# Performance work log

Hardware: AMD Instinct MI355X
Metric: run time of the kernel (lower is better)

The kernel has to match this reference:

```python
import jax, jax.numpy as jnp
import numpy as np

NEG_SLOPE = 0.01  # nn.LeakyReLU default

def leaky_relu(x):
    return jnp.where(x >= 0, x, NEG_SLOPE * x)

def setup_inputs() -> dict:
    key = jax.random.key(0)
    ks = jax.random.split(key, 10)
    N, D, H = 8192, 1447, 64
    s_in = 1.0 / np.sqrt(D)
    s_h = 1.0 / np.sqrt(H)
    return {
        "x":   jax.random.normal(ks[0], (N, D), dtype=jnp.float32),
        # fullyConnect: Linear(D -> H)
        "W_fc": jax.random.uniform(ks[1], (H, D), jnp.float32, -s_in, s_in),
        "b_fc": jax.random.uniform(ks[2], (H,), jnp.float32, -s_in, s_in),
        # transformation: Linear(H -> H)
        "W_tr": jax.random.uniform(ks[3], (H, H), jnp.float32, -s_h, s_h),
        "b_tr": jax.random.uniform(ks[4], (H,), jnp.float32, -s_h, s_h),
        # attention vector a: [2H, 1] ~ randn (nn.Parameter(torch.randn(...)))
        "a":    jax.random.normal(ks[5], (2 * H, 1), dtype=jnp.float32),
        # fc: Linear(H -> H)
        "W_f":  jax.random.uniform(ks[6], (H, H), jnp.float32, -s_h, s_h),
        "b_f":  jax.random.uniform(ks[7], (H,), jnp.float32, -s_h, s_h),
        # fc_out: Linear(H -> 1)
        "W_o":  jax.random.uniform(ks[8], (1, H), jnp.float32, -s_h, s_h),
        "b_o":  jax.random.uniform(ks[9], (1,), jnp.float32, -s_h, s_h),
    }

def reference(x, W_fc, b_fc, W_tr, b_tr, a, W_f, b_f, W_o, b_o):
    H = W_fc.shape[0]
    # hidden = leaky_relu(fullyConnect(x))                      [N, H]
    h = leaky_relu(x @ W_fc.T + b_fc)
    # attention: t = transformation(h); score[i,j] = a^T [t_j ; t_i]
    # (e_x[i,j]=t_j, e_y[i,j]=t_i in the torch code) -> separable broadcast-add
    t = h @ W_tr.T + b_tr                                       # [N, H]
    a1 = a[:H, 0]   # multiplies t_j (column index)
    a2 = a[H:, 0]   # multiplies t_i (row index)
    scores = (t @ a2)[:, None] + (t @ a1)[None, :]              # [N, N]
    att = jax.nn.softmax(leaky_relu(scores), axis=1)            # softmax over j
    # aggregate + residual
    h = att @ h + h                                             # [N, H]
    h = leaky_relu(h @ W_f.T + b_f)
    ans = (h @ W_o.T + b_o).squeeze(-1)                         # [N]
    return ans
```

## Files before the change

### kernel.cpp

```cpp
#include <hip/hip_runtime.h>

#define NROW 8192
#define DIM  1447
#define HD   64
#define NCH  48
#define LD65 65

typedef __attribute__((ext_vector_type(8))) short bf16x8;
typedef __attribute__((ext_vector_type(4))) float f32x4;
typedef float f32x4u __attribute__((ext_vector_type(4), aligned(4)));

__device__ __forceinline__ float lrelu(float v) { return v >= 0.f ? v : 0.01f * v; }

__device__ __forceinline__ unsigned short f2bf(float f) {
  unsigned u = __float_as_uint(f);
  u = u + 0x7fffu + ((u >> 16) & 1u);
  return (unsigned short)(u >> 16);
}
__device__ __forceinline__ float bf2f(unsigned short s) {
  return __uint_as_float((unsigned)s << 16);
}

__device__ __forceinline__ unsigned enc(float f) {
  unsigned u = __float_as_uint(f);
  return (u & 0x80000000u) ? ~u : (u | 0x80000000u);
}
__device__ __forceinline__ float dec(unsigned k) {
  unsigned u = (k & 0x80000000u) ? (k & 0x7fffffffu) : ~k;
  return __uint_as_float(u);
}

__device__ __forceinline__ void cvt_frag(const float* xv, bf16x8& ah, bf16x8& al) {
  union { bf16x8 v; unsigned u[4]; } H, L;
#pragma unroll
  for (int q = 0; q < 4; ++q) {
    unsigned short h0 = f2bf(xv[2 * q]),     h1 = f2bf(xv[2 * q + 1]);
    unsigned short l0 = f2bf(xv[2 * q]     - bf2f(h0));
    unsigned short l1 = f2bf(xv[2 * q + 1] - bf2f(h1));
    H.u[q] = (unsigned)h0 | ((unsigned)h1 << 16);
    L.u[q] = (unsigned)l0 | ((unsigned)l1 << 16);
  }
  ah = H.v; al = L.v;
}

union BU { int4 i; bf16x8 v; };

__global__ void k_prep(const float* __restrict__ Wtr, const float* __restrict__ btr,
                       const float* __restrict__ a, const float* __restrict__ Wfc,
                       float* __restrict__ u12, unsigned* __restrict__ m1slot,
                       unsigned short* __restrict__ WhS, unsigned short* __restrict__ WlS) {
  int t = threadIdx.x;
  int b = blockIdx.x;
  if (b == 0) {
    if (t < 64) {
      float u1 = 0.f, u2 = 0.f;
      for (int o = 0; o < 64; ++o) {
        float w = Wtr[o * 64 + t];
        u1 += w * a[o];
        u2 += w * a[64 + o];
      }
      u12[t] = u1; u12[64 + t] = u2;
      if (t == 0) {
        float c1 = 0.f, c2 = 0.f;
        for (int o = 0; o < 64; ++o) { c1 += btr[o] * a[o]; c2 += btr[o] * a[64 + o]; }
        u12[128] = c1; u12[129] = c2;
        *m1slot = 0u;
      }
    }
  } else {
    int wi = (b - 1) * 256 + t;
    int cg = wi / (NCH * 64);
    int rem = wi - cg * (NCH * 64);
    int s = rem >> 6;
    int l = rem & 63;
    int col = cg * 16 + (l & 15);
    int k0 = s * 32 + (l >> 4) * 8;
    unsigned short hv[8], lv[8];
#pragma unroll
    for (int e = 0; e < 8; ++e) {
      int k = k0 + e;
      float v = (k < DIM) ? Wfc[(size_t)col * DIM + k] : 0.f;
      unsigned short hi = f2bf(v);
      hv[e] = hi;
      lv[e] = f2bf(v - bf2f(hi));
    }
    size_t base = (size_t)wi * 8;
#pragma unroll
    for (int e = 0; e < 8; ++e) { WhS[base + e] = hv[e]; WlS[base + e] = lv[e]; }
  }
}

__global__ __launch_bounds__(256, 2) void k_gemm(const float* __restrict__ x,
    const unsigned short* __restrict__ WhS, const unsigned short* __restrict__ WlS,
    const float* __restrict__ bfc, const float* __restrict__ u12,
    float* __restrict__ h, float* __restrict__ s1, float* __restrict__ s2,
    unsigned* __restrict__ m1slot) {
  __shared__ float Pd1[16][4], Pd2[16][4];
  int t = threadIdx.x;
  int cg = t >> 6;
  int l = t & 63;
  int l15 = l & 15, l4 = l >> 4;
  int R0 = blockIdx.x * 16;
  int ko = l4 * 8;

  const float* xrow = x + (size_t)(R0 + l15) * DIM;
  const unsigned short* whp = WhS + (((size_t)cg * NCH) << 9) + (l << 3);
  const unsigned short* wlp = WlS + (((size_t)cg * NCH) << 9) + (l << 3);

  f32x4 acc = {0.f, 0.f, 0.f, 0.f};

  for (int s = 0; s < 45; ++s) {
    f32x4u x0 = *(const f32x4u*)(xrow + s * 32 + ko);
    f32x4u x1 = *(const f32x4u*)(xrow + s * 32 + ko + 4);
    float xv[8] = {x0[0], x0[1], x0[2], x0[3], x1[0], x1[1], x1[2], x1[3]};
    bf16x8 ah, al;
    cvt_frag(xv, ah, al);
    BU bh, bl;
    bh.i = *(const int4*)(whp + ((size_t)s << 9));
    bl.i = *(const int4*)(wlp + ((size_t)s << 9));
    acc = __builtin_amdgcn_mfma_f32_16x16x32_bf16(ah, bh.v, acc, 0, 0, 0);
    acc = __builtin_amdgcn_mfma_f32_16x16x32_bf16(ah, bl.v, acc, 0, 0, 0);
    acc = __builtin_amdgcn_mfma_f32_16x16x32_bf16(al, bh.v, acc, 0, 0, 0);
  }
  {
    float xv[8];
    int k0 = 45 * 32 + ko;
#pragma unroll
    for (int e = 0; e < 8; ++e) xv[e] = (k0 + e < DIM) ? xrow[k0 + e] : 0.f;
    bf16x8 ah, al;
    cvt_frag(xv, ah, al);
    BU bh, bl;
    bh.i = *(const int4*)(whp + ((size_t)45 << 9));
    bl.i = *(const int4*)(wlp + ((size_t)45 << 9));
    acc = __builtin_amdgcn_mfma_f32_16x16x32_bf16(ah, bh.v, acc, 0, 0, 0);
    acc = __builtin_amdgcn_mfma_f32_16x16x32_bf16(ah, bl.v, acc, 0, 0, 0);
    acc = __builtin_amdgcn_mfma_f32_16x16x32_bf16(al, bh.v, acc, 0, 0, 0);
  }

  int col = cg * 16 + l15;
  float bb = bfc[col];
  float u1c = u12[col], u2c = u12[64 + col];
#pragma unroll
  for (int r = 0; r < 4; ++r) {
    int rl = l4 * 4 + r;
    float hv = lrelu(acc[r] + bb);
    h[(size_t)(R0 + rl) * HD + col] = hv;
    float d1 = hv * u1c, d2 = hv * u2c;
    d1 += __shfl_xor(d1, 1); d1 += __shfl_xor(d1, 2);
    d1 += __shfl_xor(d1, 4); d1 += __shfl_xor(d1, 8);
    d2 += __shfl_xor(d2, 1); d2 += __shfl_xor(d2, 2);
    d2 += __shfl_xor(d2, 4); d2 += __shfl_xor(d2, 8);
    if (l15 == 0) { Pd1[rl][cg] = d1; Pd2[rl][cg] = d2; }
  }
  __syncthreads();
  if (t < 16) {
    float d1 = Pd1[t][0] + Pd1[t][1] + Pd1[t][2] + Pd1[t][3] + u12[128];
    float d2 = Pd2[t][0] + Pd2[t][1] + Pd2[t][2] + Pd2[t][3] + u12[129];
    int gr = R0 + t;
    s1[gr] = d1;
    s2[gr] = d2;
    float m = d1;
    m = fmaxf(m, __shfl_xor(m, 1));
    m = fmaxf(m, __shfl_xor(m, 2));
    m = fmaxf(m, __shfl_xor(m, 4));
    m = fmaxf(m, __shfl_xor(m, 8));
    if (t == 0) atomicMax(m1slot, enc(m));
  }
}

__global__ __launch_bounds__(512) void k_sort(const float* __restrict__ s1,
                                              float* __restrict__ s1s,
                                              int* __restrict__ inv) {
  __shared__ unsigned long long keys[NROW];
  __shared__ int lcnt[32];
  int t = threadIdx.x;
#pragma unroll
  for (int i = 0; i < 16; ++i) {
    int j = i * 512 + t;
    keys[j] = ((unsigned long long)enc(s1[j]) << 13) | (unsigned)j;
  }
  if (t < 32) lcnt[t] = 0;
  __syncthreads();
  int jb = blockIdx.x * 32 + (t & 7) * 4;
  unsigned long long k0 = keys[jb], k1 = keys[jb + 1], k2 = keys[jb + 2], k3 = keys[jb + 3];
  int g = t >> 3;
  int c0 = 0, c1 = 0, c2 = 0, c3 = 0;
#pragma unroll 8
  for (int e = 0; e < 128; ++e) {
    unsigned long long v = keys[g * 128 + ((e + g) & 127)];
    c0 += (v < k0); c1 += (v < k1); c2 += (v < k2); c3 += (v < k3);
  }
  int js = (t & 7) * 4;
  atomicAdd(&lcnt[js], c0);
  atomicAdd(&lcnt[js + 1], c1);
  atomicAdd(&lcnt[js + 2], c2);
  atomicAdd(&lcnt[js + 3], c3);
  __syncthreads();
  if (t < 32) {
    int r = lcnt[t];
    int j = blockIdx.x * 32 + t;
    inv[r] = j;
    s1s[r] = s1[j];
  }
}

__global__ __launch_bounds__(256) void k_trans(const float* __restrict__ h,
                                               const int* __restrict__ inv,
                                               float* __restrict__ hsT) {
  __shared__ float tile[64][65];
  int t = threadIdx.x;
  int r0 = blockIdx.x * 64;
  int rr = t >> 2;
  int cseg = (t & 3) * 16;
  int j = inv[r0 + rr];
#pragma unroll
  for (int q = 0; q < 4; ++q) {
    float4 v = *(const float4*)&h[(size_t)j * HD + cseg + q * 4];
    tile[rr][cseg + q * 4]     = v.x;
    tile[rr][cseg + q * 4 + 1] = v.y;
    tile[rr][cseg + q * 4 + 2] = v.z;
    tile[rr][cseg + q * 4 + 3] = v.w;
  }
  __syncthreads();
  int c = t >> 2;
  int rseg = (t & 3) * 16;
#pragma unroll
  for (int e = 0; e < 16; e += 4) {
    int r = rseg + e;
    float4 v = make_float4(tile[r][c], tile[r + 1][c], tile[r + 2][c], tile[r + 3][c]);
    *(float4*)&hsT[(size_t)c * NROW + r0 + r] = v;
  }
}

__global__ __launch_bounds__(512) void k_scan(const float* __restrict__ s1s,
                                              const float* __restrict__ hsT,
                                              const unsigned* __restrict__ m1slot,
                                              float* __restrict__ SufA,
                                              float* __restrict__ PreB) {
  int t = threadIdx.x;
  int c = blockIdx.x % 65;
  int br = blockIdx.x / 65;
  float M1 = dec(*m1slot);
  const float* hc = hsT + (size_t)c * NROW;
  int qb = t * 16;
  int base = br ? qb : (NROW - 16 - qb);
  float sarr[16], harr[16];
#pragma unroll
  for (int m = 0; m < 4; ++m) {
    float4 v = *(const float4*)&s1s[base + m * 4];
    sarr[m * 4] = v.x; sarr[m * 4 + 1] = v.y; sarr[m * 4 + 2] = v.z; sarr[m * 4 + 3] = v.w;
  }
  if (c < 64) {
#pragma unroll
    for (int m = 0; m < 4; ++m) {
      float4 v = *(const float4*)&hc[base + m * 4];
      harr[m * 4] = v.x; harr[m * 4 + 1] = v.y; harr[m * 4 + 2] = v.z; harr[m * 4 + 3] = v.w;
    }
  } else {
#pragma unroll
    for (int m = 0; m < 16; ++m) harr[m] = 1.0f;
  }
  float vals[16];
#pragma unroll
  for (int e = 0; e < 16; ++e) {
    int ridx = br ? e : (15 - e);
    float s = sarr[ridx];
    float w = br ? __expf(0.01f * s) : __expf(s - M1);
    vals[e] = w * harr[ridx];
  }
  float sum = 0.f;
#pragma unroll
  for (int e = 0; e < 16; ++e) sum += vals[e];
  int lane = t & 63, wid = t >> 6;
  float sc = sum;
#pragma unroll
  for (int off = 1; off < 64; off <<= 1) {
    float o = __shfl_up(sc, off);
    if (lane >= off) sc += o;
  }
  __shared__ float wt[8];
  if (lane == 63) wt[wid] = sc;
  __syncthreads();
  float woff = 0.f;
#pragma unroll
  for (int w = 0; w < 8; ++w)
    if (w < wid) woff += wt[w];
  float p = __shfl_up(sc, 1);
  float run = woff + (lane ? p : 0.f);
  if (br) {
#pragma unroll
    for (int e = 0; e < 16; ++e) {
      PreB[(size_t)(qb + e) * LD65 + c] = run;
      run += vals[e];
    }
    if (t == 511) PreB[(size_t)NROW * LD65 + c] = run;
  } else {
#pragma unroll
    for (int e = 0; e < 16; ++e) {
      run += vals[e];
      SufA[(size_t)(NROW - 1 - (qb + e)) * LD65 + c] = run;
    }
    if (t == 0) SufA[(size_t)NROW * LD65 + c] = 0.f;
  }
}

__global__ __launch_bounds__(256) void k_final(const float* __restrict__ h,
    const float* __restrict__ s1s, const float* __restrict__ s2,
    const float* __restrict__ SufA, const float* __restrict__ PreB,
    const unsigned* __restrict__ m1slot, const float* __restrict__ Wf,
    const float* __restrict__ bf, const float* __restrict__ Wo,
    const float* __restrict__ bo, float* __restrict__ out) {
  int t = threadIdx.x;
  int lane = t & 63, wid = t >> 6;
  __shared__ float coarse[64];
  if (t < 64) coarse[t] = s1s[t * 128];
  __syncthreads();
  float4 wf[16];
  const float4* wrow = (const float4*)(Wf + (size_t)lane * HD);
#pragma unroll
  for (int q = 0; q < 16; ++q) wf[q] = wrow[q];
  float bfl = bf[lane], wol = Wo[lane], bo0 = bo[0];
  float M1 = dec(*m1slot);
  float myc = coarse[lane];

  for (int rr = 0; rr < 8; ++rr) {
    int i = blockIdx.x * 32 + wid * 8 + rr;
    float s2i = s2[i];
    float th = -s2i;
    float z = s2i + M1;
    float mi = lrelu(z);
    float cA = __expf(z - mi);
    float cB = __expf(0.01f * s2i - mi);
    int n1 = __popcll(__ballot(myc < th));
    int cnt = 0;
    if (n1 > 0) {
      int L = (n1 - 1) * 128;
      float v2 = s1s[L + 1 + 2 * lane];
      int n2 = __popcll(__ballot(v2 < th));
      cnt = L + 2 * n2;
      if (cnt < NROW && s1s[cnt] < th) cnt++;
    }
    const float* ra = SufA + (size_t)cnt * LD65;
    const float* rb = PreB + (size_t)cnt * LD65;
    float vA = ra[lane], vB = rb[lane];
    float zA = ra[64],  zB = rb[64];
    float Z = cA * zA + cB * zB;
    float h2 = (cA * vA + cB * vB) / Z + h[(size_t)i * HD + lane];
    float acc = bfl;
#pragma unroll
    for (int q = 0; q < 16; ++q) {
      float4 wv = wf[q];
      int c = q * 4;
      acc += wv.x * __shfl(h2, c) + wv.y * __shfl(h2, c + 1) +
             wv.z * __shfl(h2, c + 2) + wv.w * __shfl(h2, c + 3);
    }
    float h3 = lrelu(acc);
    float pv = h3 * wol;
#pragma unroll
    for (int off = 32; off > 0; off >>= 1) pv += __shfl_xor(pv, off);
    if (lane == 0) out[i] = pv + bo0;
  }
}

extern "C" void kernel_launch(void* const* d_in, const int* in_sizes, int n_in,
                              void* d_out, int out_size, void* d_ws, size_t ws_size,
                              hipStream_t stream) {
  const float* x   = (const float*)d_in[0];
  const float* Wfc = (const float*)d_in[1];
  const float* bfc = (const float*)d_in[2];
  const float* Wtr = (const float*)d_in[3];
  const float* btr = (const float*)d_in[4];
  const float* a   = (const float*)d_in[5];
  const float* Wf  = (const float*)d_in[6];
  const float* bf  = (const float*)d_in[7];
  const float* Wo  = (const float*)d_in[8];
  const float* bo  = (const float*)d_in[9];
  float* out = (float*)d_out;

  char* w = (char*)d_ws;
  size_t off = 0;
  auto alloc = [&](size_t bytes) -> void* {
    void* p = w + off;
    off = (off + bytes + 255) & ~(size_t)255;
    return p;
  };
  float* h      = (float*)alloc((size_t)NROW * HD * 4);
  float* s1     = (float*)alloc(NROW * 4);
  float* s2     = (float*)alloc(NROW * 4);
  float* u12    = (float*)alloc(130 * 4);
  unsigned* m1  = (unsigned*)alloc(4);
  int* inv      = (int*)alloc(NROW * 4);
  float* s1s    = (float*)alloc(NROW * 4);
  unsigned short* WhS = (unsigned short*)alloc((size_t)4 * NCH * 64 * 8 * 2);
  unsigned short* WlS = (unsigned short*)alloc((size_t)4 * NCH * 64 * 8 * 2);
  float* hsT    = (float*)alloc((size_t)HD * NROW * 4);
  float* SufA   = (float*)alloc((size_t)(NROW + 1) * LD65 * 4);
  float* PreB   = (float*)alloc((size_t)(NROW + 1) * LD65 * 4);
  (void)in_sizes; (void)n_in; (void)out_size; (void)ws_size;

  k_prep<<<1 + (4 * NCH * 64) / 256, 256, 0, stream>>>(Wtr, btr, a, Wfc, u12, m1, WhS, WlS);
  k_gemm<<<NROW / 16, 256, 0, stream>>>(x, WhS, WlS, bfc, u12, h, s1, s2, m1);
  k_sort<<<NROW / 32, 512, 0, stream>>>(s1, s1s, inv);
  k_trans<<<NROW / 64, 256, 0, stream>>>(h, inv, hsT);
  k_scan<<<130, 512, 0, stream>>>(s1s, hsT, m1, SufA, PreB);
  k_final<<<NROW / 32, 256, 0, stream>>>(h, s1s, s2, SufA, PreB, m1, Wf, bf, Wo, bo, out);
}
```

Baseline: 79.59 us.

## Stage x through LDS with double buffering, split K across waves, rework sort and transpose

The input GEMM now stages x tiles through shared memory in double-buffered chunks of 128 columns, using coalesced loads. It splits the K dimension across two wave groups in 512-thread blocks and reduces their partial accumulators through LDS. The rank sort drops 64-bit keys and instead compares floats with an index tiebreak, using float4 LDS reads and shuffle reductions in place of shared atomics. The transpose kernel moves to smaller 32-row tiles with twice as many blocks. Together these aim at better memory coalescing and higher occupancy, at the cost of extra LDS traffic and barriers.

```diff
diff --git a/kernel.cpp b/kernel.cpp
--- a/kernel.cpp
+++ b/kernel.cpp
@@ -3,7 +3,8 @@
 #define NROW 8192
 #define DIM  1447
 #define HD   64
-#define NCH  48
+#define NST  46
+#define NCHK 12
 #define LD65 65
 
 typedef __attribute__((ext_vector_type(8))) short bf16x8;
@@ -28,19 +29,6 @@
 __device__ __forceinline__ float dec(unsigned k) {
   unsigned u = (k & 0x80000000u) ? (k & 0x7fffffffu) : ~k;
   return __uint_as_float(u);
-}
-
-__device__ __forceinline__ void cvt_frag(const float* xv, bf16x8& ah, bf16x8& al) {
-  union { bf16x8 v; unsigned u[4]; } H, L;
-#pragma unroll
-  for (int q = 0; q < 4; ++q) {
-    unsigned short h0 = f2bf(xv[2 * q]),     h1 = f2bf(xv[2 * q + 1]);
-    unsigned short l0 = f2bf(xv[2 * q]     - bf2f(h0));
-    unsigned short l1 = f2bf(xv[2 * q + 1] - bf2f(h1));
-    H.u[q] = (unsigned)h0 | ((unsigned)h1 << 16);
-    L.u[q] = (unsigned)l0 | ((unsigned)l1 << 16);
-  }
-  ah = H.v; al = L.v;
 }
 
 union BU { int4 i; bf16x8 v; };
@@ -69,88 +57,131 @@
     }
   } else {
     int wi = (b - 1) * 256 + t;
-    int cg = wi / (NCH * 64);
-    int rem = wi - cg * (NCH * 64);
-    int s = rem >> 6;
-    int l = rem & 63;
-    int col = cg * 16 + (l & 15);
-    int k0 = s * 32 + (l >> 4) * 8;
-    unsigned short hv[8], lv[8];
-#pragma unroll
-    for (int e = 0; e < 8; ++e) {
-      int k = k0 + e;
-      float v = (k < DIM) ? Wfc[(size_t)col * DIM + k] : 0.f;
-      unsigned short hi = f2bf(v);
-      hv[e] = hi;
-      lv[e] = f2bf(v - bf2f(hi));
-    }
-    size_t base = (size_t)wi * 8;
-#pragma unroll
-    for (int e = 0; e < 8; ++e) { WhS[base + e] = hv[e]; WlS[base + e] = lv[e]; }
-  }
-}
-
-__global__ __launch_bounds__(256, 2) void k_gemm(const float* __restrict__ x,
+    if (wi < 4 * NST * 64) {
+      int cg = wi / (NST * 64);
+      int rem = wi - cg * (NST * 64);
+      int s = rem >> 6;
+      int l = rem & 63;
+      int col = cg * 16 + (l & 15);
+      int k0 = s * 32 + (l >> 4) * 8;
+      unsigned short hv[8], lv[8];
+#pragma unroll
+      for (int e = 0; e < 8; ++e) {
+        int k = k0 + e;
+        float v = (k < DIM) ? Wfc[(size_t)col * DIM + k] : 0.f;
+        unsigned short hi = f2bf(v);
+        hv[e] = hi;
+        lv[e] = f2bf(v - bf2f(hi));
+      }
+      size_t base = (size_t)wi * 8;
+#pragma unroll
+      for (int e = 0; e < 8; ++e) { WhS[base + e] = hv[e]; WlS[base + e] = lv[e]; }
+    }
+  }
+}
+
+__global__ __launch_bounds__(512, 4) void k_gemm(const float* __restrict__ x,
     const unsigned short* __restrict__ WhS, const unsigned short* __restrict__ WlS,
     const float* __restrict__ bfc, const float* __restrict__ u12,
     float* __restrict__ h, float* __restrict__ s1, float* __restrict__ s2,
     unsigned* __restrict__ m1slot) {
+  __shared__ unsigned short XH[2][16][136], XL[2][16][136];
+  __shared__ float Pacc[4][16][17];
   __shared__ float Pd1[16][4], Pd2[16][4];
   int t = threadIdx.x;
-  int cg = t >> 6;
+  int wv = t >> 6;
   int l = t & 63;
   int l15 = l & 15, l4 = l >> 4;
+  int cg = wv & 3;
+  int kh = wv >> 2;
   int R0 = blockIdx.x * 16;
-  int ko = l4 * 8;
-
-  const float* xrow = x + (size_t)(R0 + l15) * DIM;
-  const unsigned short* whp = WhS + (((size_t)cg * NCH) << 9) + (l << 3);
-  const unsigned short* wlp = WlS + (((size_t)cg * NCH) << 9) + (l << 3);
+  int srow = t >> 5;
+  int skl = (t & 31) * 4;
+
+  const float* xst = x + (size_t)(R0 + srow) * DIM;
+  const unsigned short* whp = WhS + (((size_t)cg * NST) << 9) + (l << 3);
+  const unsigned short* wlp = WlS + (((size_t)cg * NST) << 9) + (l << 3);
+
+  float xr0, xr1, xr2, xr3;
+
+#define STLOAD(C)                                                          \
+  do {                                                                     \
+    int kg_ = (C) * 128 + skl;                                             \
+    if ((C) < 11) {                                                        \
+      f32x4u v_ = *(const f32x4u*)(xst + kg_);                             \
+      xr0 = v_[0]; xr1 = v_[1]; xr2 = v_[2]; xr3 = v_[3];                  \
+    } else {                                                               \
+      xr0 = (kg_     < DIM) ? xst[kg_]     : 0.f;                          \
+      xr1 = (kg_ + 1 < DIM) ? xst[kg_ + 1] : 0.f;                          \
+      xr2 = (kg_ + 2 < DIM) ? xst[kg_ + 2] : 0.f;                          \
+      xr3 = (kg_ + 3 < DIM) ? xst[kg_ + 3] : 0.f;                          \
+    }                                                                      \
+  } while (0)
+
+#define STWRITE(B)                                                         \
+  do {                                                                     \
+    unsigned short h0_ = f2bf(xr0), h1_ = f2bf(xr1),                       \
+                   h2_ = f2bf(xr2), h3_ = f2bf(xr3);                       \
+    unsigned short m0_ = f2bf(xr0 - bf2f(h0_)), m1_ = f2bf(xr1 - bf2f(h1_)), \
+                   m2_ = f2bf(xr2 - bf2f(h2_)), m3_ = f2bf(xr3 - bf2f(h3_)); \
+    uint2 ph_, pl_;                                                        \
+    ph_.x = (unsigned)h0_ | ((unsigned)h1_ << 16);                         \
+    ph_.y = (unsigned)h2_ | ((unsigned)h3_ << 16);                         \
+    pl_.x = (unsigned)m0_ | ((unsigned)m1_ << 16);                         \
+    pl_.y = (unsigned)m2_ | ((unsigned)m3_ << 16);                         \
+    *(uint2*)&XH[B][srow][skl] = ph_;                                      \
+    *(uint2*)&XL[B][srow][skl] = pl_;                                      \
+  } while (0)
 
   f32x4 acc = {0.f, 0.f, 0.f, 0.f};
 
-  for (int s = 0; s < 45; ++s) {
-    f32x4u x0 = *(const f32x4u*)(xrow + s * 32 + ko);
-    f32x4u x1 = *(const f32x4u*)(xrow + s * 32 + ko + 4);
-    float xv[8] = {x0[0], x0[1], x0[2], x0[3], x1[0], x1[1], x1[2], x1[3]};
-    bf16x8 ah, al;
-    cvt_frag(xv, ah, al);
-    BU bh, bl;
-    bh.i = *(const int4*)(whp + ((size_t)s << 9));
-    bl.i = *(const int4*)(wlp + ((size_t)s << 9));
-    acc = __builtin_amdgcn_mfma_f32_16x16x32_bf16(ah, bh.v, acc, 0, 0, 0);
-    acc = __builtin_amdgcn_mfma_f32_16x16x32_bf16(ah, bl.v, acc, 0, 0, 0);
-    acc = __builtin_amdgcn_mfma_f32_16x16x32_bf16(al, bh.v, acc, 0, 0, 0);
-  }
-  {
-    float xv[8];
-    int k0 = 45 * 32 + ko;
-#pragma unroll
-    for (int e = 0; e < 8; ++e) xv[e] = (k0 + e < DIM) ? xrow[k0 + e] : 0.f;
-    bf16x8 ah, al;
-    cvt_frag(xv, ah, al);
-    BU bh, bl;
-    bh.i = *(const int4*)(whp + ((size_t)45 << 9));
-    bl.i = *(const int4*)(wlp + ((size_t)45 << 9));
-    acc = __builtin_amdgcn_mfma_f32_16x16x32_bf16(ah, bh.v, acc, 0, 0, 0);
-    acc = __builtin_amdgcn_mfma_f32_16x16x32_bf16(ah, bl.v, acc, 0, 0, 0);
-    acc = __builtin_amdgcn_mfma_f32_16x16x32_bf16(al, bh.v, acc, 0, 0, 0);
-  }
-
-  int col = cg * 16 + l15;
-  float bb = bfc[col];
-  float u1c = u12[col], u2c = u12[64 + col];
-#pragma unroll
-  for (int r = 0; r < 4; ++r) {
-    int rl = l4 * 4 + r;
-    float hv = lrelu(acc[r] + bb);
-    h[(size_t)(R0 + rl) * HD + col] = hv;
-    float d1 = hv * u1c, d2 = hv * u2c;
-    d1 += __shfl_xor(d1, 1); d1 += __shfl_xor(d1, 2);
-    d1 += __shfl_xor(d1, 4); d1 += __shfl_xor(d1, 8);
-    d2 += __shfl_xor(d2, 1); d2 += __shfl_xor(d2, 2);
-    d2 += __shfl_xor(d2, 4); d2 += __shfl_xor(d2, 8);
-    if (l15 == 0) { Pd1[rl][cg] = d1; Pd2[rl][cg] = d2; }
+  STLOAD(0);
+  STWRITE(0);
+  __syncthreads();
+
+  for (int c = 0; c < NCHK; ++c) {
+    int buf = c & 1;
+    if (c + 1 < NCHK) STLOAD(c + 1);
+    int nloc = (c == 11) ? 1 : 2;
+    for (int ii = 0; ii < nloc; ++ii) {
+      int sl = kh + ii * 2;
+      int sg = c * 4 + sl;
+      BU bh, bl;
+      bh.i = *(const int4*)(whp + ((size_t)sg << 9));
+      bl.i = *(const int4*)(wlp + ((size_t)sg << 9));
+      bf16x8 ah = *(const bf16x8*)&XH[buf][l15][sl * 32 + l4 * 8];
+      bf16x8 al = *(const bf16x8*)&XL[buf][l15][sl * 32 + l4 * 8];
+      acc = __builtin_amdgcn_mfma_f32_16x16x32_bf16(ah, bh.v, acc, 0, 0, 0);
+      acc = __builtin_amdgcn_mfma_f32_16x16x32_bf16(ah, bl.v, acc, 0, 0, 0);
+      acc = __builtin_amdgcn_mfma_f32_16x16x32_bf16(al, bh.v, acc, 0, 0, 0);
+    }
+    if (c + 1 < NCHK) STWRITE(buf ^ 1);
+    __syncthreads();
+  }
+#undef STLOAD
+#undef STWRITE
+
+  if (kh == 1) {
+#pragma unroll
+    for (int r = 0; r < 4; ++r) Pacc[cg][l4 * 4 + r][l15] = acc[r];
+  }
+  __syncthreads();
+  if (kh == 0) {
+    int col = cg * 16 + l15;
+    float bb = bfc[col];
+    float u1c = u12[col], u2c = u12[64 + col];
+#pragma unroll
+    for (int r = 0; r < 4; ++r) {
+      int rl = l4 * 4 + r;
+      float hv = lrelu(acc[r] + Pacc[cg][rl][l15] + bb);
+      h[(size_t)(R0 + rl) * HD + col] = hv;
+      float d1 = hv * u1c, d2 = hv * u2c;
+      d1 += __shfl_xor(d1, 1); d1 += __shfl_xor(d1, 2);
+      d1 += __shfl_xor(d1, 4); d1 += __shfl_xor(d1, 8);
+      d2 += __shfl_xor(d2, 1); d2 += __shfl_xor(d2, 2);
+      d2 += __shfl_xor(d2, 4); d2 += __shfl_xor(d2, 8);
+      if (l15 == 0) { Pd1[rl][cg] = d1; Pd2[rl][cg] = d2; }
+    }
   }
   __syncthreads();
   if (t < 16) {
@@ -171,50 +202,43 @@
 __global__ __launch_bounds__(512) void k_sort(const float* __restrict__ s1,
                                               float* __restrict__ s1s,
                                               int* __restrict__ inv) {
-  __shared__ unsigned long long keys[NROW];
-  __shared__ int lcnt[32];
-  int t = threadIdx.x;
-#pragma unroll
-  for (int i = 0; i < 16; ++i) {
-    int j = i * 512 + t;
-    keys[j] = ((unsigned long long)enc(s1[j]) << 13) | (unsigned)j;
-  }
-  if (t < 32) lcnt[t] = 0;
-  __syncthreads();
-  int jb = blockIdx.x * 32 + (t & 7) * 4;
-  unsigned long long k0 = keys[jb], k1 = keys[jb + 1], k2 = keys[jb + 2], k3 = keys[jb + 3];
-  int g = t >> 3;
-  int c0 = 0, c1 = 0, c2 = 0, c3 = 0;
-#pragma unroll 8
+  __shared__ alignas(16) float sv[NROW];
+  int t = threadIdx.x;
+#pragma unroll
+  for (int i = 0; i < 16; ++i) sv[i * 512 + t] = s1[i * 512 + t];
+  __syncthreads();
+  int jl = t >> 4, sub = t & 15;
+  int j = blockIdx.x * 32 + jl;
+  float my = sv[j];
+  int base = sub * 512;
+  int cnt = 0;
+#pragma unroll 4
   for (int e = 0; e < 128; ++e) {
-    unsigned long long v = keys[g * 128 + ((e + g) & 127)];
-    c0 += (v < k0); c1 += (v < k1); c2 += (v < k2); c3 += (v < k3);
-  }
-  int js = (t & 7) * 4;
-  atomicAdd(&lcnt[js], c0);
-  atomicAdd(&lcnt[js + 1], c1);
-  atomicAdd(&lcnt[js + 2], c2);
-  atomicAdd(&lcnt[js + 3], c3);
-  __syncthreads();
-  if (t < 32) {
-    int r = lcnt[t];
-    int j = blockIdx.x * 32 + t;
-    inv[r] = j;
-    s1s[r] = s1[j];
-  }
+    int off = ((e + sub * 9) & 127) * 4;
+    int i0 = base + off;
+    float4 v = *(const float4*)&sv[i0];
+    cnt += (v.x < my) + (v.y < my) + (v.z < my) + (v.w < my);
+    cnt += (v.x == my && i0 < j) + (v.y == my && i0 + 1 < j) +
+           (v.z == my && i0 + 2 < j) + (v.w == my && i0 + 3 < j);
+  }
+  cnt += __shfl_xor(cnt, 1);
+  cnt += __shfl_xor(cnt, 2);
+  cnt += __shfl_xor(cnt, 4);
+  cnt += __shfl_xor(cnt, 8);
+  if (sub == 0) { inv[cnt] = j; s1s[cnt] = my; }
 }
 
 __global__ __launch_bounds__(256) void k_trans(const float* __restrict__ h,
                                                const int* __restrict__ inv,
                                                float* __restrict__ hsT) {
-  __shared__ float tile[64][65];
-  int t = threadIdx.x;
-  int r0 = blockIdx.x * 64;
-  int rr = t >> 2;
-  int cseg = (t & 3) * 16;
+  __shared__ float tile[32][65];
+  int t = threadIdx.x;
+  int r0 = blockIdx.x * 32;
+  int rr = t >> 3;
+  int cseg = (t & 7) * 8;
   int j = inv[r0 + rr];
 #pragma unroll
-  for (int q = 0; q < 4; ++q) {
+  for (int q = 0; q < 2; ++q) {
     float4 v = *(const float4*)&h[(size_t)j * HD + cseg + q * 4];
     tile[rr][cseg + q * 4]     = v.x;
     tile[rr][cseg + q * 4 + 1] = v.y;
@@ -223,9 +247,9 @@
   }
   __syncthreads();
   int c = t >> 2;
-  int rseg = (t & 3) * 16;
-#pragma unroll
-  for (int e = 0; e < 16; e += 4) {
+  int rseg = (t & 3) * 8;
+#pragma unroll
+  for (int e = 0; e < 8; e += 4) {
     int r = rseg + e;
     float4 v = make_float4(tile[r][c], tile[r + 1][c], tile[r + 2][c], tile[r + 3][c]);
     *(float4*)&hsT[(size_t)c * NROW + r0 + r] = v;
@@ -391,17 +415,17 @@
   unsigned* m1  = (unsigned*)alloc(4);
   int* inv      = (int*)alloc(NROW * 4);
   float* s1s    = (float*)alloc(NROW * 4);
-  unsigned short* WhS = (unsigned short*)alloc((size_t)4 * NCH * 64 * 8 * 2);
-  unsigned short* WlS = (unsigned short*)alloc((size_t)4 * NCH * 64 * 8 * 2);
+  unsigned short* WhS = (unsigned short*)alloc((size_t)4 * NST * 64 * 8 * 2);
+  unsigned short* WlS = (unsigned short*)alloc((size_t)4 * NST * 64 * 8 * 2);
   float* hsT    = (float*)alloc((size_t)HD * NROW * 4);
   float* SufA   = (float*)alloc((size_t)(NROW + 1) * LD65 * 4);
   float* PreB   = (float*)alloc((size_t)(NROW + 1) * LD65 * 4);
   (void)in_sizes; (void)n_in; (void)out_size; (void)ws_size;
 
-  k_prep<<<1 + (4 * NCH * 64) / 256, 256, 0, stream>>>(Wtr, btr, a, Wfc, u12, m1, WhS, WlS);
-  k_gemm<<<NROW / 16, 256, 0, stream>>>(x, WhS, WlS, bfc, u12, h, s1, s2, m1);
+  k_prep<<<1 + (4 * NST * 64 + 255) / 256, 256, 0, stream>>>(Wtr, btr, a, Wfc, u12, m1, WhS, WlS);
+  k_gemm<<<NROW / 16, 512, 0, stream>>>(x, WhS, WlS, bfc, u12, h, s1, s2, m1);
   k_sort<<<NROW / 32, 512, 0, stream>>>(s1, s1s, inv);
-  k_trans<<<NROW / 64, 256, 0, stream>>>(h, inv, hsT);
+  k_trans<<<NROW / 32, 256, 0, stream>>>(h, inv, hsT);
   k_scan<<<130, 512, 0, stream>>>(s1s, hsT, m1, SufA, PreB);
   k_final<<<NROW / 32, 256, 0, stream>>>(h, s1s, s2, SufA, PreB, m1, Wf, bf, Wo, bo, out);
 }
```

Result: slower. 104.0 us (+30.6%).
